# Performance work log

Hardware: AMD Instinct MI355X
Metric: run time of the kernel (lower is better)

Reference implementation:

```python
import jax, jax.numpy as jnp
import numpy as np

SIGMA_DATA = 16.0
ALPHA_BOND = 1.0


def safe_norm(x, axis=-1):
    # L2 norm with zero (sub)gradient at 0, matching torch.norm's behavior
    sq = jnp.sum(x * x, axis=axis)
    n = jnp.sqrt(jnp.where(sq > 0, sq, 1.0))
    return jnp.where(sq > 0, n, 0.0)


def weighted_rigid_align(x_l, xGT_l, w_l):
    # Aligns x_l onto xGT_l's frame (Kabsch with weights); output is detached.
    wm = w_l[..., None]                                   # [B,N,1]
    denom = jnp.sum(wm, axis=1, keepdims=True)
    mu = jnp.sum(wm * x_l, axis=1, keepdims=True) / denom
    muGT = jnp.sum(wm * xGT_l, axis=1, keepdims=True) / denom
    xc = x_l - mu
    xGTc = xGT_l - muGT
    # M = (w * xGT_c)^T @ x_c  -> [B,3,3]
    M = jnp.einsum('bni,bnj->bij', wm * xGTc, xc)
    U, S, Vh = jnp.linalg.svd(M)
    R = U @ Vh
    det = jnp.linalg.det(R)
    Fm = jnp.array([[1.0, 0.0, 0.0], [0.0, 1.0, 0.0], [0.0, 0.0, -1.0]], dtype=R.dtype)
    Rfix = jnp.einsum('bij,jk,bkl->bil', U, Fm, Vh)
    R = jnp.where(det[:, None, None] < 0, Rfix, R)
    xalign = xc @ jnp.swapaxes(R, -1, -2) + muGT
    return jax.lax.stop_gradient(xalign)


def diffusion_loss(xpred_l, xGT_l, ht, w_l):
    # Align ground truth onto prediction (note arg order in original forward)
    xGT_aligned = weighted_rigid_align(xGT_l, xpred_l, w_l)
    loss = jnp.sum(safe_norm(xpred_l - xGT_aligned) * w_l) / jnp.sum(w_l)
    if ALPHA_BOND > 0:
        w_pair = w_l[:, :, None] * w_l[:, None, :]                 # [B,N,N]
        d_pred = safe_norm(xpred_l[:, :, None] - xpred_l[:, None]) # [B,N,N]
        d_gt = safe_norm(xGT_l[:, :, None] - xGT_l[:, None])       # [B,N,N]
        L_bond = w_pair * (d_pred - d_gt) ** 2
        loss = loss + ALPHA_BOND * jnp.sum(L_bond) / jnp.sum(w_pair)
    return (ht ** 2 + SIGMA_DATA ** 2) / (ht + SIGMA_DATA) ** 2 * loss


def setup_inputs() -> dict:
    key = jax.random.key(0)
    k1, k2, k3, k4 = jax.random.split(key, 4)
    B, N = 4, 2048
    xpred_l = jax.random.normal(k1, (B, N, 3), dtype=jnp.float32) * 10.0
    xGT_l = jax.random.normal(k2, (B, N, 3), dtype=jnp.float32) * 10.0
    ht = jax.random.uniform(k3, (B,), dtype=jnp.float32, minval=0.1, maxval=4.0)
    w_l = jax.random.uniform(k4, (B, N), dtype=jnp.float32, minval=0.1, maxval=1.0)
    return {"xpred_l": xpred_l, "xGT_l": xGT_l, "ht": ht, "w_l": w_l}


def reference(xpred_l, xGT_l, ht, w_l):
    return diffusion_loss(xpred_l, xGT_l, ht, w_l)
```

## Files before the change

### kernel.cpp

```cpp
#include <hip/hip_runtime.h>
#include <math.h>


#define RT 256
#define CT 128
#define MAXB 8

__global__ __launch_bounds__(RT, 4)
void k_main(const float* __restrict__ pred, const float* __restrict__ gt,
            const float* __restrict__ ht, const float* __restrict__ w,
            float* __restrict__ out, double* __restrict__ ws,
            int N, int B, unsigned total, unsigned ngroups) {
    const int b    = blockIdx.z;
    const int bx   = blockIdx.x;
    const int r0   = bx * RT;
    const int c0   = blockIdx.y * CT;
    const int tid  = threadIdx.x;
    const int lane = tid & 63, wave = tid >> 6;
    const int GX   = gridDim.x;
    const unsigned linear = (blockIdx.z * gridDim.y + blockIdx.y) * GX + blockIdx.x;

    double*   statsSlot = ws;
    double*   bondSlot  = ws + (size_t)B * GX * 16;
    unsigned* cnt       = (unsigned*)(bondSlot + total);

    const float* p  = pred + (size_t)b * N * 3;
    const float* g  = gt   + (size_t)b * N * 3;
    const float* wb = w    + (size_t)b * N;

    __shared__ float4 sp4[CT], sg4[CT];
    __shared__ double shred[4][16];

    const int  n      = r0 + tid;
    const bool row_ok = (n < N);
    float px=0.f,py=0.f,pz=0.f,gx=0.f,gy=0.f,gz=0.f,wn=0.f;
    if (row_ok) {
        px = p[3*n]; py = p[3*n+1]; pz = p[3*n+2];
        gx = g[3*n]; gy = g[3*n+1]; gz = g[3*n+2];
        wn = wb[n];
    }

    const bool bond_active = (c0 + CT > r0 + 1) && (c0 < N);
    float bond_f = 0.0f;
    if (bond_active) {
        for (int i = tid; i < CT; i += RT) {
            int m = c0 + i;
            float4 a = make_float4(0.f,0.f,0.f,0.f), c = a;
            if (m < N) {
                a = make_float4(p[3*m], p[3*m+1], p[3*m+2], wb[m]);
                c = make_float4(g[3*m], g[3*m+1], g[3*m+2], 0.f);
            }
            sp4[i] = a; sg4[i] = c;
        }
        __syncthreads();
        if (row_ok) {
            const int cc = min(CT, N - c0);
            if (c0 >= r0 + RT) {
                #pragma unroll 4
                for (int i = 0; i < cc; i++) {
                    float4 cp = sp4[i], cg = sg4[i];
                    float dxp=px-cp.x, dyp=py-cp.y, dzp=pz-cp.z;
                    float dxg=gx-cg.x, dyg=gy-cg.y, dzg=gz-cg.z;
                    float dp = sqrtf(dxp*dxp+dyp*dyp+dzp*dzp);
                    float dg = sqrtf(dxg*dxg+dyg*dyg+dzg*dzg);
                    float dd = dp - dg;
                    bond_f += (wn*cp.w)*(dd*dd);
                }
            } else if (n < c0 + cc - 1) {
                #pragma unroll 4
                for (int i = 0; i < cc; i++) {
                    float4 cp = sp4[i], cg = sg4[i];
                    float dxp=px-cp.x, dyp=py-cp.y, dzp=pz-cp.z;
                    float dxg=gx-cg.x, dyg=gy-cg.y, dzg=gz-cg.z;
                    float dp = sqrtf(dxp*dxp+dyp*dyp+dzp*dzp);
                    float dg = sqrtf(dxg*dxg+dyg*dyg+dzg*dzg);
                    float dd = dp - dg;
                    float t  = (wn*cp.w)*(dd*dd);
                    bond_f += (c0 + i > n) ? t : 0.0f;
                }
            }
        }
    }
    bond_f *= 2.0f;

    if (blockIdx.y == 0) {
        double wd=wn, pxd=px,pyd=py,pzd=pz, gxd=gx,gyd=gy,gzd=gz;
        double st[16] = {wd, wd*pxd, wd*pyd, wd*pzd, wd*gxd, wd*gyd, wd*gzd,
                         wd*pxd*gxd, wd*pxd*gyd, wd*pxd*gzd,
                         wd*pyd*gxd, wd*pyd*gyd, wd*pyd*gzd,
                         wd*pzd*gxd, wd*pzd*gyd, wd*pzd*gzd};
        #pragma unroll
        for (int off = 32; off > 0; off >>= 1) {
            #pragma unroll
            for (int k = 0; k < 16; k++) st[k] += __shfl_down(st[k], off, 64);
        }
        if (lane == 0) {
            #pragma unroll
            for (int k = 0; k < 16; k++) shred[wave][k] = st[k];
        }
        __syncthreads();
        if (tid < 16)
            __hip_atomic_store(&statsSlot[((size_t)b*GX + bx)*16 + tid],
                               shred[0][tid]+shred[1][tid]+shred[2][tid]+shred[3][tid],
                               __ATOMIC_RELAXED, __HIP_MEMORY_SCOPE_AGENT);
        __syncthreads();
    }

    double bd = (double)bond_f;
    #pragma unroll
    for (int off = 32; off > 0; off >>= 1) bd += __shfl_down(bd, off, 64);
    if (lane == 0) shred[wave][0] = bd;
    __syncthreads();
    if (tid == 0)
        __hip_atomic_store(&bondSlot[linear],
                           shred[0][0]+shred[1][0]+shred[2][0]+shred[3][0],
                           __ATOMIC_RELAXED, __HIP_MEMORY_SCOPE_AGENT);

    __shared__ unsigned s_old;
    __syncthreads();
    if (tid == 0) {
        unsigned grp   = linear >> 5;
        unsigned gsize = min(32u, total - (grp << 5));
        unsigned og = __hip_atomic_fetch_add(&cnt[grp * 32], 1u,
                                             __ATOMIC_RELAXED, __HIP_MEMORY_SCOPE_AGENT);
        unsigned ov = 0xFFFFFFFFu;
        if (og == gsize - 1u)
            ov = __hip_atomic_fetch_add(&cnt[ngroups * 32], 1u,
                                        __ATOMIC_RELAXED, __HIP_MEMORY_SCOPE_AGENT);
        s_old = ov;
    }
    __syncthreads();
    if (s_old != ngroups - 1u) return;

    __shared__ double sstat[MAXB][16];
    __shared__ float  Rf[MAXB][15];
    __shared__ double Wd[MAXB];
    __shared__ double s_bond, s_loss;

    if (tid < B * 16) {
        int bb = tid >> 4, k = tid & 15;
        double acc = 0.0;
        for (int j = 0; j < GX; j++)
            acc += __hip_atomic_load(&statsSlot[((size_t)bb*GX + j)*16 + k],
                                     __ATOMIC_RELAXED, __HIP_MEMORY_SCOPE_AGENT);
        sstat[bb][k] = acc;
    }

    double bsum = 0.0;
    for (unsigned i = tid; i < total; i += RT)
        bsum += __hip_atomic_load(&bondSlot[i], __ATOMIC_RELAXED,
                                  __HIP_MEMORY_SCOPE_AGENT);
    #pragma unroll
    for (int off = 32; off > 0; off >>= 1) bsum += __shfl_down(bsum, off, 64);
    if (lane == 0) shred[wave][1] = bsum;
    __syncthreads();
    if (tid == 0) s_bond = shred[0][1]+shred[1][1]+shred[2][1]+shred[3][1];

    if (tid < B) {
        const double* s = sstat[tid];
        double W = s[0];
        double mupd[3] = { s[1]/W, s[2]/W, s[3]/W };
        double mugd[3] = { s[4]/W, s[5]/W, s[6]/W };
        double Md[3][3];
        double mmax = 0.0;
        for (int i = 0; i < 3; i++)
            for (int j = 0; j < 3; j++) {
                Md[i][j] = s[7 + i*3 + j] - W * mupd[i] * mugd[j];
                mmax = fmax(mmax, fabs(Md[i][j]));
            }
        double detM = Md[0][0]*(Md[1][1]*Md[2][2] - Md[1][2]*Md[2][1])
                    - Md[0][1]*(Md[1][0]*Md[2][2] - Md[1][2]*Md[2][0])
                    + Md[0][2]*(Md[1][0]*Md[2][1] - Md[1][1]*Md[2][0]);
        float sg2 = (detM < 0.0) ? -1.0f : 1.0f;

        float M[3][3];
        float inv_mmax = (mmax > 0.0) ? (float)(1.0 / mmax) : 0.0f;
        for (int i = 0; i < 3; i++)
            for (int j = 0; j < 3; j++) M[i][j] = (float)Md[i][j] * inv_mmax;

        float A[3][3];
        for (int i = 0; i < 3; i++)
            for (int j = 0; j < 3; j++) {
                float t = 0.0f;
                for (int k = 0; k < 3; k++) t += M[k][i] * M[k][j];
                A[i][j] = t;
            }
        float V[3][3] = {{1,0,0},{0,1,0},{0,0,1}};
        for (int sweep = 0; sweep < 6; sweep++) {
            for (int pq = 0; pq < 3; pq++) {
                int pp_ = (pq == 2) ? 1 : 0;
                int qq_ = (pq == 0) ? 1 : 2;
                float apq = A[pp_][qq_];
                if (fabsf(apq) < 1e-30f) continue;
                float app = A[pp_][pp_], aqq = A[qq_][qq_];
                float theta = (aqq - app) / (2.0f * apq);
                float t = copysignf(1.0f, theta) / (fabsf(theta) + sqrtf(theta*theta + 1.0f));
                float cj = 1.0f / sqrtf(t*t + 1.0f), sn = t * cj;
                A[pp_][pp_] = app - t * apq;
                A[qq_][qq_] = aqq + t * apq;
                A[pp_][qq_] = A[qq_][pp_] = 0.0f;
                int r = 3 - pp_ - qq_;
                float arp = A[r][pp_], arq = A[r][qq_];
                A[r][pp_] = A[pp_][r] = cj*arp - sn*arq;
                A[r][qq_] = A[qq_][r] = sn*arp + cj*arq;
                for (int rr = 0; rr < 3; rr++) {
                    float vp = V[rr][pp_], vq = V[rr][qq_];
                    V[rr][pp_] = cj*vp - sn*vq;
                    V[rr][qq_] = sn*vp + cj*vq;
                }
            }
        }
        float d[3] = { A[0][0], A[1][1], A[2][2] };
        int idx[3] = {0, 1, 2};
        for (int i = 0; i < 2; i++)
            for (int j = i + 1; j < 3; j++)
                if (d[idx[j]] > d[idx[i]]) { int tt = idx[i]; idx[i] = idx[j]; idx[j] = tt; }
        float u[3][3], v[3][3];
        for (int i = 0; i < 3; i++) {
            int c_ = idx[i];
            float sv = sqrtf(fmaxf(d[c_], 0.0f));
            float inv = (sv > 1e-7f) ? 1.0f / sv : 0.0f;
            for (int r = 0; r < 3; r++) v[i][r] = V[r][c_];
            for (int r = 0; r < 3; r++) {
                float t = 0.0f;
                for (int k = 0; k < 3; k++) t += M[r][k] * v[i][k];
                u[i][r] = t * inv;
            }
        }
        for (int r = 0; r < 3; r++)
            for (int cc2 = 0; cc2 < 3; cc2++)
                Rf[tid][r*3+cc2] = u[0][r]*v[0][cc2] + u[1][r]*v[1][cc2]
                                 + sg2 * u[2][r]*v[2][cc2];
        for (int i = 0; i < 3; i++) Rf[tid][9 + i]  = (float)mupd[i];
        for (int i = 0; i < 3; i++) Rf[tid][12 + i] = (float)mugd[i];
        Wd[tid] = W;
    }
    __syncthreads();

    double al = 0.0;
    for (int bb = 0; bb < B; bb++) {
        float R0=Rf[bb][0], R1=Rf[bb][1], R2=Rf[bb][2];
        float R3=Rf[bb][3], R4=Rf[bb][4], R5=Rf[bb][5];
        float R6=Rf[bb][6], R7=Rf[bb][7], R8=Rf[bb][8];
        float mp0=Rf[bb][9],  mp1=Rf[bb][10], mp2=Rf[bb][11];
        float mg0=Rf[bb][12], mg1=Rf[bb][13], mg2=Rf[bb][14];
        const float* pp  = pred + (size_t)bb * N * 3;
        const float* gg  = gt   + (size_t)bb * N * 3;
        const float* wwb = w    + (size_t)bb * N;
        for (int nn = tid; nn < N; nn += RT) {
            float x0 = gg[3*nn]-mg0, x1 = gg[3*nn+1]-mg1, x2 = gg[3*nn+2]-mg2;
            float ax = fmaf(R0,x0, fmaf(R1,x1, fmaf(R2,x2, mp0)));
            float ay = fmaf(R3,x0, fmaf(R4,x1, fmaf(R5,x2, mp1)));
            float az = fmaf(R6,x0, fmaf(R7,x1, fmaf(R8,x2, mp2)));
            float ex = pp[3*nn]-ax, ey = pp[3*nn+1]-ay, ez = pp[3*nn+2]-az;
            float sq = ex*ex + ey*ey + ez*ez;
            al += (double)(wwb[nn] * sqrtf(sq));
        }
    }
    #pragma unroll
    for (int off = 32; off > 0; off >>= 1) al += __shfl_down(al, off, 64);
    if (lane == 0) shred[wave][2] = al;
    __syncthreads();
    if (tid == 0) {
        double at = shred[0][2]+shred[1][2]+shred[2][2]+shred[3][2];
        double tw = 0.0, twp = 0.0;
        for (int i = 0; i < B; i++) { double W = Wd[i]; tw += W; twp += W*W; }
        s_loss = at / tw + s_bond / twp;
    }
    __syncthreads();
    if (tid < B) {
        double h = (double)ht[tid];
        out[tid] = (float)(((h*h + 256.0) / ((h + 16.0)*(h + 16.0))) * s_loss);
    }
}

extern "C" void kernel_launch(void* const* d_in, const int* in_sizes, int n_in,
                              void* d_out, int out_size, void* d_ws, size_t ws_size,
                              hipStream_t stream) {
    const float* pred = (const float*)d_in[0];
    const float* gt   = (const float*)d_in[1];
    const float* ht   = (const float*)d_in[2];
    const float* w    = (const float*)d_in[3];
    int B = in_sizes[2];
    int N = in_sizes[3] / B;
    double* ws = (double*)d_ws;
    float* out = (float*)d_out;

    int gx = (N + RT - 1) / RT;
    int gy = (N + CT - 1) / CT;
    unsigned total   = (unsigned)(gx * gy * B);
    unsigned ngroups = (total + 31u) >> 5;
    size_t cnt_off   = ((size_t)B * gx * 16 + total) * sizeof(double);
    size_t cnt_bytes = ((size_t)ngroups * 32 + 1) * sizeof(unsigned);

    hipMemsetAsync((char*)d_ws + cnt_off, 0, cnt_bytes, stream);
    k_main<<<dim3(gx, gy, B), dim3(RT), 0, stream>>>(pred, gt, ht, w, out, ws,
                                                     N, B, total, ngroups);
}
```

Measured before the change: 106.1 us.

## Split stats+SVD into a pre-kernel and fold alignment loss into pair blocks

Adds a small pre-kernel (one 1024-thread block per batch) that computes the weighted moments and the 3x3 SVD rotation, so the main pairwise kernel can compute the per-row alignment residual in its column-0 blocks. This removes the serial tail where the last block redid the SVD and rescanned all B*N points. The column tile is halved to produce more blocks, and the hierarchical counter is replaced by a single atomic counter. The cost is an extra kernel launch with a very low-occupancy grid running before the pair work, plus more contention on that one counter.

```diff
diff --git a/kernel.cpp b/kernel.cpp
--- a/kernel.cpp
+++ b/kernel.cpp
@@ -3,14 +3,136 @@
 
 
 #define RT 256
-#define CT 128
+#define CT 64
+#define ST 1024
 #define MAXB 8
 
+__global__ __launch_bounds__(ST, 1)
+void k_stats_svd(const float* __restrict__ pred, const float* __restrict__ gt,
+                 const float* __restrict__ w, double* __restrict__ ws, int N) {
+    const int b    = blockIdx.x;
+    const int tid  = threadIdx.x;
+    const int lane = tid & 63, wave = tid >> 6;
+    const float* p  = pred + (size_t)b * N * 3;
+    const float* g  = gt   + (size_t)b * N * 3;
+    const float* wb = w    + (size_t)b * N;
+
+    double acc[16];
+    #pragma unroll
+    for (int i = 0; i < 16; i++) acc[i] = 0.0;
+    for (int n = tid; n < N; n += ST) {
+        double wn = wb[n];
+        double px = p[3*n], py = p[3*n+1], pz = p[3*n+2];
+        double gx = g[3*n], gy = g[3*n+1], gz = g[3*n+2];
+        acc[0] += wn;
+        acc[1] += wn*px; acc[2] += wn*py; acc[3] += wn*pz;
+        acc[4] += wn*gx; acc[5] += wn*gy; acc[6] += wn*gz;
+        acc[7]  += wn*px*gx; acc[8]  += wn*px*gy; acc[9]  += wn*px*gz;
+        acc[10] += wn*py*gx; acc[11] += wn*py*gy; acc[12] += wn*py*gz;
+        acc[13] += wn*pz*gx; acc[14] += wn*pz*gy; acc[15] += wn*pz*gz;
+    }
+    #pragma unroll
+    for (int off = 32; off > 0; off >>= 1) {
+        #pragma unroll
+        for (int i = 0; i < 16; i++) acc[i] += __shfl_down(acc[i], off, 64);
+    }
+    __shared__ double sh[16][16];
+    if (lane == 0) {
+        #pragma unroll
+        for (int i = 0; i < 16; i++) sh[wave][i] = acc[i];
+    }
+    __syncthreads();
+    __shared__ double s[16];
+    if (tid < 16) {
+        double t = 0.0;
+        for (int wv = 0; wv < ST/64; wv++) t += sh[wv][tid];
+        s[tid] = t;
+    }
+    __syncthreads();
+    if (tid != 0) return;
+
+    double W = s[0];
+    double mupd[3] = { s[1]/W, s[2]/W, s[3]/W };
+    double mugd[3] = { s[4]/W, s[5]/W, s[6]/W };
+    double Md[3][3]; double mmax = 0.0;
+    for (int i = 0; i < 3; i++)
+        for (int j = 0; j < 3; j++) {
+            Md[i][j] = s[7 + i*3 + j] - W * mupd[i] * mugd[j];
+            mmax = fmax(mmax, fabs(Md[i][j]));
+        }
+    double detM = Md[0][0]*(Md[1][1]*Md[2][2] - Md[1][2]*Md[2][1])
+                - Md[0][1]*(Md[1][0]*Md[2][2] - Md[1][2]*Md[2][0])
+                + Md[0][2]*(Md[1][0]*Md[2][1] - Md[1][1]*Md[2][0]);
+    float sg2 = (detM < 0.0) ? -1.0f : 1.0f;
+
+    float M[3][3];
+    float inv_mmax = (mmax > 0.0) ? (float)(1.0 / mmax) : 0.0f;
+    for (int i = 0; i < 3; i++)
+        for (int j = 0; j < 3; j++) M[i][j] = (float)Md[i][j] * inv_mmax;
+    float A[3][3];
+    for (int i = 0; i < 3; i++)
+        for (int j = 0; j < 3; j++) {
+            float t = 0.0f;
+            for (int k = 0; k < 3; k++) t += M[k][i] * M[k][j];
+            A[i][j] = t;
+        }
+    float V[3][3] = {{1,0,0},{0,1,0},{0,0,1}};
+    for (int sweep = 0; sweep < 6; sweep++) {
+        for (int pq = 0; pq < 3; pq++) {
+            int pp_ = (pq == 2) ? 1 : 0;
+            int qq_ = (pq == 0) ? 1 : 2;
+            float apq = A[pp_][qq_];
+            if (fabsf(apq) < 1e-30f) continue;
+            float app = A[pp_][pp_], aqq = A[qq_][qq_];
+            float theta = (aqq - app) / (2.0f * apq);
+            float t = copysignf(1.0f, theta) / (fabsf(theta) + sqrtf(theta*theta + 1.0f));
+            float cj = 1.0f / sqrtf(t*t + 1.0f), sn = t * cj;
+            A[pp_][pp_] = app - t * apq;
+            A[qq_][qq_] = aqq + t * apq;
+            A[pp_][qq_] = A[qq_][pp_] = 0.0f;
+            int r = 3 - pp_ - qq_;
+            float arp = A[r][pp_], arq = A[r][qq_];
+            A[r][pp_] = A[pp_][r] = cj*arp - sn*arq;
+            A[r][qq_] = A[qq_][r] = sn*arp + cj*arq;
+            for (int rr = 0; rr < 3; rr++) {
+                float vp = V[rr][pp_], vq = V[rr][qq_];
+                V[rr][pp_] = cj*vp - sn*vq;
+                V[rr][qq_] = sn*vp + cj*vq;
+            }
+        }
+    }
+    float d[3] = { A[0][0], A[1][1], A[2][2] };
+    int idx[3] = {0, 1, 2};
+    for (int i = 0; i < 2; i++)
+        for (int j = i + 1; j < 3; j++)
+            if (d[idx[j]] > d[idx[i]]) { int tt = idx[i]; idx[i] = idx[j]; idx[j] = tt; }
+    float u[3][3], v[3][3];
+    for (int i = 0; i < 3; i++) {
+        int c_ = idx[i];
+        float sv = sqrtf(fmaxf(d[c_], 0.0f));
+        float inv = (sv > 1e-7f) ? 1.0f / sv : 0.0f;
+        for (int r = 0; r < 3; r++) v[i][r] = V[r][c_];
+        for (int r = 0; r < 3; r++) {
+            float t = 0.0f;
+            for (int k = 0; k < 3; k++) t += M[r][k] * v[i][k];
+            u[i][r] = t * inv;
+        }
+    }
+    double* o = ws + (size_t)b * 16;
+    for (int r = 0; r < 3; r++)
+        for (int c2 = 0; c2 < 3; c2++)
+            o[r*3+c2] = (double)(u[0][r]*v[0][c2] + u[1][r]*v[1][c2]
+                                 + sg2 * u[2][r]*v[2][c2]);
+    for (int i = 0; i < 3; i++) o[9 + i]  = mupd[i];
+    for (int i = 0; i < 3; i++) o[12 + i] = mugd[i];
+    o[15] = W;
+}
+
 __global__ __launch_bounds__(RT, 4)
-void k_main(const float* __restrict__ pred, const float* __restrict__ gt,
+void k_pair(const float* __restrict__ pred, const float* __restrict__ gt,
             const float* __restrict__ ht, const float* __restrict__ w,
             float* __restrict__ out, double* __restrict__ ws,
-            int N, int B, unsigned total, unsigned ngroups) {
+            int N, int B, unsigned total) {
     const int b    = blockIdx.z;
     const int bx   = blockIdx.x;
     const int r0   = bx * RT;
@@ -20,16 +142,17 @@
     const int GX   = gridDim.x;
     const unsigned linear = (blockIdx.z * gridDim.y + blockIdx.y) * GX + blockIdx.x;
 
-    double*   statsSlot = ws;
-    double*   bondSlot  = ws + (size_t)B * GX * 16;
-    unsigned* cnt       = (unsigned*)(bondSlot + total);
+    double*   Rrow      = ws;
+    double*   bondSlot  = ws + (size_t)B * 16;
+    double*   alignSlot = bondSlot + total;
+    unsigned* cnt       = (unsigned*)(alignSlot + (size_t)B * GX);
 
     const float* p  = pred + (size_t)b * N * 3;
     const float* g  = gt   + (size_t)b * N * 3;
     const float* wb = w    + (size_t)b * N;
 
     __shared__ float4 sp4[CT], sg4[CT];
-    __shared__ double shred[4][16];
+    __shared__ double shred[4][2];
 
     const int  n      = r0 + tid;
     const bool row_ok = (n < N);
@@ -83,189 +206,74 @@
     }
     bond_f *= 2.0f;
 
-    if (blockIdx.y == 0) {
-        double wd=wn, pxd=px,pyd=py,pzd=pz, gxd=gx,gyd=gy,gzd=gz;
-        double st[16] = {wd, wd*pxd, wd*pyd, wd*pzd, wd*gxd, wd*gyd, wd*gzd,
-                         wd*pxd*gxd, wd*pxd*gyd, wd*pxd*gzd,
-                         wd*pyd*gxd, wd*pyd*gyd, wd*pyd*gzd,
-                         wd*pzd*gxd, wd*pzd*gyd, wd*pzd*gzd};
-        #pragma unroll
-        for (int off = 32; off > 0; off >>= 1) {
-            #pragma unroll
-            for (int k = 0; k < 16; k++) st[k] += __shfl_down(st[k], off, 64);
-        }
-        if (lane == 0) {
-            #pragma unroll
-            for (int k = 0; k < 16; k++) shred[wave][k] = st[k];
-        }
-        __syncthreads();
-        if (tid < 16)
-            __hip_atomic_store(&statsSlot[((size_t)b*GX + bx)*16 + tid],
-                               shred[0][tid]+shred[1][tid]+shred[2][tid]+shred[3][tid],
-                               __ATOMIC_RELAXED, __HIP_MEMORY_SCOPE_AGENT);
-        __syncthreads();
+    double align_d = 0.0;
+    if (blockIdx.y == 0 && row_ok) {
+        const double* o = Rrow + (size_t)b * 16;
+        float R0=(float)o[0], R1=(float)o[1], R2=(float)o[2];
+        float R3=(float)o[3], R4=(float)o[4], R5=(float)o[5];
+        float R6=(float)o[6], R7=(float)o[7], R8=(float)o[8];
+        float mp0=(float)o[9],  mp1=(float)o[10], mp2=(float)o[11];
+        float mg0=(float)o[12], mg1=(float)o[13], mg2=(float)o[14];
+        float x0 = gx-mg0, x1 = gy-mg1, x2 = gz-mg2;
+        float ax = fmaf(R0,x0, fmaf(R1,x1, fmaf(R2,x2, mp0)));
+        float ay = fmaf(R3,x0, fmaf(R4,x1, fmaf(R5,x2, mp1)));
+        float az = fmaf(R6,x0, fmaf(R7,x1, fmaf(R8,x2, mp2)));
+        float ex = px-ax, ey = py-ay, ez = pz-az;
+        float sq = ex*ex + ey*ey + ez*ez;
+        align_d = (double)(wn * sqrtf(sq));
     }
 
     double bd = (double)bond_f;
     #pragma unroll
-    for (int off = 32; off > 0; off >>= 1) bd += __shfl_down(bd, off, 64);
-    if (lane == 0) shred[wave][0] = bd;
-    __syncthreads();
-    if (tid == 0)
+    for (int off = 32; off > 0; off >>= 1) {
+        bd      += __shfl_down(bd, off, 64);
+        align_d += __shfl_down(align_d, off, 64);
+    }
+    if (bond_active) __syncthreads();
+    if (lane == 0) { shred[wave][0] = bd; shred[wave][1] = align_d; }
+    __syncthreads();
+    if (tid == 0) {
         __hip_atomic_store(&bondSlot[linear],
                            shred[0][0]+shred[1][0]+shred[2][0]+shred[3][0],
                            __ATOMIC_RELAXED, __HIP_MEMORY_SCOPE_AGENT);
+        if (blockIdx.y == 0)
+            __hip_atomic_store(&alignSlot[(size_t)b*GX + bx],
+                               shred[0][1]+shred[1][1]+shred[2][1]+shred[3][1],
+                               __ATOMIC_RELAXED, __HIP_MEMORY_SCOPE_AGENT);
+    }
 
     __shared__ unsigned s_old;
     __syncthreads();
-    if (tid == 0) {
-        unsigned grp   = linear >> 5;
-        unsigned gsize = min(32u, total - (grp << 5));
-        unsigned og = __hip_atomic_fetch_add(&cnt[grp * 32], 1u,
-                                             __ATOMIC_RELAXED, __HIP_MEMORY_SCOPE_AGENT);
-        unsigned ov = 0xFFFFFFFFu;
-        if (og == gsize - 1u)
-            ov = __hip_atomic_fetch_add(&cnt[ngroups * 32], 1u,
-                                        __ATOMIC_RELAXED, __HIP_MEMORY_SCOPE_AGENT);
-        s_old = ov;
-    }
-    __syncthreads();
-    if (s_old != ngroups - 1u) return;
-
-    __shared__ double sstat[MAXB][16];
-    __shared__ float  Rf[MAXB][15];
-    __shared__ double Wd[MAXB];
-    __shared__ double s_bond, s_loss;
-
-    if (tid < B * 16) {
-        int bb = tid >> 4, k = tid & 15;
-        double acc = 0.0;
-        for (int j = 0; j < GX; j++)
-            acc += __hip_atomic_load(&statsSlot[((size_t)bb*GX + j)*16 + k],
-                                     __ATOMIC_RELAXED, __HIP_MEMORY_SCOPE_AGENT);
-        sstat[bb][k] = acc;
-    }
+    if (tid == 0) s_old = __hip_atomic_fetch_add(cnt, 1u, __ATOMIC_RELAXED,
+                                                 __HIP_MEMORY_SCOPE_AGENT);
+    __syncthreads();
+    if (s_old != total - 1u) return;
 
     double bsum = 0.0;
     for (unsigned i = tid; i < total; i += RT)
         bsum += __hip_atomic_load(&bondSlot[i], __ATOMIC_RELAXED,
                                   __HIP_MEMORY_SCOPE_AGENT);
+    double asum = 0.0;
+    for (unsigned i = tid; i < (unsigned)(B*GX); i += RT)
+        asum += __hip_atomic_load(&alignSlot[i], __ATOMIC_RELAXED,
+                                  __HIP_MEMORY_SCOPE_AGENT);
     #pragma unroll
-    for (int off = 32; off > 0; off >>= 1) bsum += __shfl_down(bsum, off, 64);
-    if (lane == 0) shred[wave][1] = bsum;
-    __syncthreads();
-    if (tid == 0) s_bond = shred[0][1]+shred[1][1]+shred[2][1]+shred[3][1];
-
-    if (tid < B) {
-        const double* s = sstat[tid];
-        double W = s[0];
-        double mupd[3] = { s[1]/W, s[2]/W, s[3]/W };
-        double mugd[3] = { s[4]/W, s[5]/W, s[6]/W };
-        double Md[3][3];
-        double mmax = 0.0;
-        for (int i = 0; i < 3; i++)
-            for (int j = 0; j < 3; j++) {
-                Md[i][j] = s[7 + i*3 + j] - W * mupd[i] * mugd[j];
-                mmax = fmax(mmax, fabs(Md[i][j]));
-            }
-        double detM = Md[0][0]*(Md[1][1]*Md[2][2] - Md[1][2]*Md[2][1])
-                    - Md[0][1]*(Md[1][0]*Md[2][2] - Md[1][2]*Md[2][0])
-                    + Md[0][2]*(Md[1][0]*Md[2][1] - Md[1][1]*Md[2][0]);
-        float sg2 = (detM < 0.0) ? -1.0f : 1.0f;
-
-        float M[3][3];
-        float inv_mmax = (mmax > 0.0) ? (float)(1.0 / mmax) : 0.0f;
-        for (int i = 0; i < 3; i++)
-            for (int j = 0; j < 3; j++) M[i][j] = (float)Md[i][j] * inv_mmax;
-
-        float A[3][3];
-        for (int i = 0; i < 3; i++)
-            for (int j = 0; j < 3; j++) {
-                float t = 0.0f;
-                for (int k = 0; k < 3; k++) t += M[k][i] * M[k][j];
-                A[i][j] = t;
-            }
-        float V[3][3] = {{1,0,0},{0,1,0},{0,0,1}};
-        for (int sweep = 0; sweep < 6; sweep++) {
-            for (int pq = 0; pq < 3; pq++) {
-                int pp_ = (pq == 2) ? 1 : 0;
-                int qq_ = (pq == 0) ? 1 : 2;
-                float apq = A[pp_][qq_];
-                if (fabsf(apq) < 1e-30f) continue;
-                float app = A[pp_][pp_], aqq = A[qq_][qq_];
-                float theta = (aqq - app) / (2.0f * apq);
-                float t = copysignf(1.0f, theta) / (fabsf(theta) + sqrtf(theta*theta + 1.0f));
-                float cj = 1.0f / sqrtf(t*t + 1.0f), sn = t * cj;
-                A[pp_][pp_] = app - t * apq;
-                A[qq_][qq_] = aqq + t * apq;
-                A[pp_][qq_] = A[qq_][pp_] = 0.0f;
-                int r = 3 - pp_ - qq_;
-                float arp = A[r][pp_], arq = A[r][qq_];
-                A[r][pp_] = A[pp_][r] = cj*arp - sn*arq;
-                A[r][qq_] = A[qq_][r] = sn*arp + cj*arq;
-                for (int rr = 0; rr < 3; rr++) {
-                    float vp = V[rr][pp_], vq = V[rr][qq_];
-                    V[rr][pp_] = cj*vp - sn*vq;
-                    V[rr][qq_] = sn*vp + cj*vq;
-                }
-            }
-        }
-        float d[3] = { A[0][0], A[1][1], A[2][2] };
-        int idx[3] = {0, 1, 2};
-        for (int i = 0; i < 2; i++)
-            for (int j = i + 1; j < 3; j++)
-                if (d[idx[j]] > d[idx[i]]) { int tt = idx[i]; idx[i] = idx[j]; idx[j] = tt; }
-        float u[3][3], v[3][3];
-        for (int i = 0; i < 3; i++) {
-            int c_ = idx[i];
-            float sv = sqrtf(fmaxf(d[c_], 0.0f));
-            float inv = (sv > 1e-7f) ? 1.0f / sv : 0.0f;
-            for (int r = 0; r < 3; r++) v[i][r] = V[r][c_];
-            for (int r = 0; r < 3; r++) {
-                float t = 0.0f;
-                for (int k = 0; k < 3; k++) t += M[r][k] * v[i][k];
-                u[i][r] = t * inv;
-            }
-        }
-        for (int r = 0; r < 3; r++)
-            for (int cc2 = 0; cc2 < 3; cc2++)
-                Rf[tid][r*3+cc2] = u[0][r]*v[0][cc2] + u[1][r]*v[1][cc2]
-                                 + sg2 * u[2][r]*v[2][cc2];
-        for (int i = 0; i < 3; i++) Rf[tid][9 + i]  = (float)mupd[i];
-        for (int i = 0; i < 3; i++) Rf[tid][12 + i] = (float)mugd[i];
-        Wd[tid] = W;
-    }
-    __syncthreads();
-
-    double al = 0.0;
-    for (int bb = 0; bb < B; bb++) {
-        float R0=Rf[bb][0], R1=Rf[bb][1], R2=Rf[bb][2];
-        float R3=Rf[bb][3], R4=Rf[bb][4], R5=Rf[bb][5];
-        float R6=Rf[bb][6], R7=Rf[bb][7], R8=Rf[bb][8];
-        float mp0=Rf[bb][9],  mp1=Rf[bb][10], mp2=Rf[bb][11];
-        float mg0=Rf[bb][12], mg1=Rf[bb][13], mg2=Rf[bb][14];
-        const float* pp  = pred + (size_t)bb * N * 3;
-        const float* gg  = gt   + (size_t)bb * N * 3;
-        const float* wwb = w    + (size_t)bb * N;
-        for (int nn = tid; nn < N; nn += RT) {
-            float x0 = gg[3*nn]-mg0, x1 = gg[3*nn+1]-mg1, x2 = gg[3*nn+2]-mg2;
-            float ax = fmaf(R0,x0, fmaf(R1,x1, fmaf(R2,x2, mp0)));
-            float ay = fmaf(R3,x0, fmaf(R4,x1, fmaf(R5,x2, mp1)));
-            float az = fmaf(R6,x0, fmaf(R7,x1, fmaf(R8,x2, mp2)));
-            float ex = pp[3*nn]-ax, ey = pp[3*nn+1]-ay, ez = pp[3*nn+2]-az;
-            float sq = ex*ex + ey*ey + ez*ez;
-            al += (double)(wwb[nn] * sqrtf(sq));
-        }
-    }
-    #pragma unroll
-    for (int off = 32; off > 0; off >>= 1) al += __shfl_down(al, off, 64);
-    if (lane == 0) shred[wave][2] = al;
-    __syncthreads();
+    for (int off = 32; off > 0; off >>= 1) {
+        bsum += __shfl_down(bsum, off, 64);
+        asum += __shfl_down(asum, off, 64);
+    }
+    if (lane == 0) { shred[wave][0] = bsum; shred[wave][1] = asum; }
+    __syncthreads();
+    __shared__ double s_loss;
     if (tid == 0) {
-        double at = shred[0][2]+shred[1][2]+shred[2][2]+shred[3][2];
+        double bt = shred[0][0]+shred[1][0]+shred[2][0]+shred[3][0];
+        double at = shred[0][1]+shred[1][1]+shred[2][1]+shred[3][1];
         double tw = 0.0, twp = 0.0;
-        for (int i = 0; i < B; i++) { double W = Wd[i]; tw += W; twp += W*W; }
-        s_loss = at / tw + s_bond / twp;
+        for (int i = 0; i < B; i++) {
+            double W = Rrow[(size_t)i*16 + 15];
+            tw += W; twp += W*W;
+        }
+        s_loss = at / tw + bt / twp;
     }
     __syncthreads();
     if (tid < B) {
@@ -288,12 +296,10 @@
 
     int gx = (N + RT - 1) / RT;
     int gy = (N + CT - 1) / CT;
-    unsigned total   = (unsigned)(gx * gy * B);
-    unsigned ngroups = (total + 31u) >> 5;
-    size_t cnt_off   = ((size_t)B * gx * 16 + total) * sizeof(double);
-    size_t cnt_bytes = ((size_t)ngroups * 32 + 1) * sizeof(unsigned);
-
-    hipMemsetAsync((char*)d_ws + cnt_off, 0, cnt_bytes, stream);
-    k_main<<<dim3(gx, gy, B), dim3(RT), 0, stream>>>(pred, gt, ht, w, out, ws,
-                                                     N, B, total, ngroups);
+    unsigned total = (unsigned)(gx * gy * B);
+    size_t cnt_off = ((size_t)B * 16 + total + (size_t)B * gx) * sizeof(double);
+
+    hipMemsetAsync((char*)d_ws + cnt_off, 0, sizeof(unsigned), stream);
+    k_stats_svd<<<dim3(B), dim3(ST), 0, stream>>>(pred, gt, w, ws, N);
+    k_pair<<<dim3(gx, gy, B), dim3(RT), 0, stream>>>(pred, gt, ht, w, out, ws, N, B, total);
 }
```

Result: no change. 105.0 us (-1.0%).
